# Performance work log

Hardware: AMD Instinct MI355X
Metric: run time of the kernel (lower is better)

## Reference

```python
import jax, jax.numpy as jnp
import numpy as np

ALPHA = 0.2  # LeakyReLU negative slope
NEG_BIG = -9e15

def setup_inputs() -> dict:
    key = jax.random.key(0)
    k1, k2, k3, k4 = jax.random.split(key, 4)
    N, F_IN, F_OUT = 8192, 128, 128
    h = jax.random.normal(k1, (N, F_IN), dtype=jnp.float32)
    adj = jax.random.randint(k2, (N, N), 0, 2, dtype=jnp.int32)
    # xavier-uniform-ish params
    W = jax.random.normal(k3, (F_IN, F_OUT), dtype=jnp.float32) * (1.0 / np.sqrt(F_IN))
    a = jax.random.normal(k4, (2 * F_OUT, 1), dtype=jnp.float32) * (1.0 / np.sqrt(2 * F_OUT))
    return {"h": h, "adj": adj, "W": W, "a": a}

def reference(h, adj, W, a):
    # Wh: [N, F_OUT]
    Wh = h @ W
    F_out = Wh.shape[1]
    # a_input @ a == (Wh @ a1)_i + (Wh @ a2)_j  (same math, no N^2*2F tensor)
    a1 = a[:F_out, 0]   # [F_OUT]
    a2 = a[F_out:, 0]   # [F_OUT]
    e = (Wh @ a1)[:, None] + (Wh @ a2)[None, :]        # [N, N]
    e = jnp.where(e >= 0, e, ALPHA * e)                # LeakyReLU(0.2)
    scores = jnp.where(adj > 0, e, NEG_BIG)
    attention = jax.nn.softmax(scores, axis=1)         # row-wise
    # dropout skipped (eval mode / training=False)
    return attention @ Wh                              # [N, F_OUT]
```

## Files before the change

kernel.cpp:

```cpp
#include <hip/hip_runtime.h>
#include <hip/hip_bf16.h>

#define N 8192
#define FD 128
#define LOG2E 1.4426950408889634f

typedef __attribute__((ext_vector_type(4))) float f4;
typedef __attribute__((ext_vector_type(4))) int i32x4;
typedef __attribute__((ext_vector_type(4))) unsigned int u32x4;
typedef __attribute__((ext_vector_type(8))) __bf16 bf16x8;

__device__ __forceinline__ unsigned short bfbits(float x){
  __bf16 b = (__bf16)x;
  return __builtin_bit_cast(unsigned short, b);
}

__global__ __launch_bounds__(256) void k12_wh(const float* __restrict__ h,
                                              const float* __restrict__ W,
                                              const float* __restrict__ a,
                                              unsigned short* __restrict__ Bsw,
                                              float* __restrict__ s1L,
                                              float* __restrict__ s2L){
  __shared__ float Wl[64*128];
  __shared__ float hT[128*33];
  int t = threadIdx.x;
  int i0 = blockIdx.x * 32;
  {
    int r  = t >> 3;
    int k0 = (t & 7) * 16;
    const f4* src = (const f4*)&h[(size_t)(i0 + r)*FD + k0];
    #pragma unroll
    for (int q = 0; q < 4; ++q){
      f4 v = src[q];
      #pragma unroll
      for (int e = 0; e < 4; ++e) hT[(k0 + q*4 + e)*33 + r] = v[e];
    }
  }
  int f0 = (t & 31) * 4;
  int r0 = (t >> 5) * 4;
  float acc[4][4] = {};
  for (int half = 0; half < 2; ++half){
    __syncthreads();
    #pragma unroll
    for (int v = 0; v < 8; ++v){
      int idx = (v*256 + t)*4;
      *(f4*)&Wl[idx] = *(const f4*)&W[half*8192 + idx];
    }
    __syncthreads();
    for (int k2 = 0; k2 < 64; ++k2){
      f4 wv = *(const f4*)&Wl[k2*FD + f0];
      f4 hv = *(const f4*)&hT[(half*64 + k2)*33 + r0];
      #pragma unroll
      for (int ri = 0; ri < 4; ++ri)
        #pragma unroll
        for (int fi = 0; fi < 4; ++fi)
          acc[ri][fi] = __builtin_fmaf(hv[ri], wv[fi], acc[ri][fi]);
    }
  }
  int jblk = blockIdx.x;
  int n  = f0 >> 4;
  int fl = f0 & 15;
  #pragma unroll
  for (int ri = 0; ri < 4; ++ri){
    int k = r0 + ri;
    size_t base = (((size_t)jblk*8 + n)*64 + ((k>>3)<<4))*8 + (k&7);
    #pragma unroll
    for (int fi = 0; fi < 4; ++fi)
      Bsw[base + (size_t)(fl + fi)*8] = bfbits(acc[ri][fi]);
  }
  f4 a1v = *(const f4*)&a[f0];
  f4 a2v = *(const f4*)&a[FD + f0];
  float p1[4], p2[4];
  #pragma unroll
  for (int ri = 0; ri < 4; ++ri){
    p1[ri] = 0.f; p2[ri] = 0.f;
    #pragma unroll
    for (int fi = 0; fi < 4; ++fi){
      p1[ri] = __builtin_fmaf(acc[ri][fi], a1v[fi], p1[ri]);
      p2[ri] = __builtin_fmaf(acc[ri][fi], a2v[fi], p2[ri]);
    }
  }
  #pragma unroll
  for (int d = 1; d < 32; d <<= 1){
    #pragma unroll
    for (int ri = 0; ri < 4; ++ri){
      p1[ri] += __shfl_xor(p1[ri], d, 32);
      p2[ri] += __shfl_xor(p2[ri], d, 32);
    }
  }
  if ((t & 31) == 0){
    #pragma unroll
    for (int ri = 0; ri < 4; ++ri){
      s1L[i0 + r0 + ri] = p1[ri] * LOG2E;
      s2L[i0 + r0 + ri] = p2[ri] * LOG2E;
    }
  }
}

__global__ __launch_bounds__(256) void k3_max(const float* __restrict__ s2L,
                                              float* __restrict__ M2L){
  __shared__ float red[4];
  int t = threadIdx.x;
  float m = -3.0e38f;
  for (int i = t; i < N; i += 256) m = fmaxf(m, s2L[i]);
  #pragma unroll
  for (int d = 1; d < 64; d <<= 1) m = fmaxf(m, __shfl_xor(m, d, 64));
  if ((t & 63) == 0) red[t >> 6] = m;
  __syncthreads();
  if (t == 0) *M2L = fmaxf(fmaxf(red[0], red[1]), fmaxf(red[2], red[3]));
}

__global__ __launch_bounds__(256,2) void k4_flash(const int* __restrict__ adj,
    const unsigned short* __restrict__ Bsw,
    const float* __restrict__ s1L, const float* __restrict__ s2L,
    const float* __restrict__ M2p,
    float* __restrict__ partial, float* __restrict__ denomp, int njc){
  __shared__ __align__(16) unsigned char bswl[2][32768];
  __shared__ __align__(16) unsigned char mknib[2][128*32];
  __shared__ __align__(16) float s2l[2][128];
  int t = threadIdx.x;
  int wv = t >> 6, lane = t & 63;
  int lrow = lane & 15, lgrp = lane >> 4;
  int bid = blockIdx.x;
  int y  = bid & (njc - 1);
  int bx = bid / njc;
  int jlen = N / njc;
  int jstart = y * jlen;
  int nmac = jlen >> 7;
  int rotm = nmac - 1;
  float M2 = *M2p;
  int i0w = bx*128 + wv*32;
  float s1a = s1L[i0w + lrow], s1b = s1L[i0w + 16 + lrow];
  float ea = s1a + M2, eb = s1b + M2;
  float maL = fmaxf(ea, 0.2f*ea);
  float mbL = fmaxf(eb, 0.2f*eb);

  f4 acc[2][8]; f4 accd[2];
  #pragma unroll
  for (int x = 0; x < 2; ++x){
    accd[x] = (f4){0.f,0.f,0.f,0.f};
    #pragma unroll
    for (int n = 0; n < 8; ++n) acc[x][n] = (f4){0.f,0.f,0.f,0.f};
  }
  u32x4 onesbits = (u32x4){0x3F803F80u,0x3F803F80u,0x3F803F80u,0x3F803F80u};
  bf16x8 ones = __builtin_bit_cast(bf16x8, onesbits);

  const i32x4* adj4 = (const i32x4*)adj;
  int sr2 = lane >> 5;
  int sj  = lane & 31;
  size_t abase = ((size_t)(bx*128 + wv*32 + sr2) * N) >> 2;

  i32x4 st[16];

  #define STAGE_BSW(jb0, b) do {                                               \
    const unsigned int* bg = (const unsigned int*)(Bsw + (size_t)((jb0) >> 5) * 4096); \
    _Pragma("unroll")                                                          \
    for (int q = 0; q < 8; ++q){                                               \
      int chunk = q*4 + wv;                                                    \
      __builtin_amdgcn_global_load_lds(                                        \
        (const __attribute__((address_space(1))) unsigned int*)(bg + (size_t)(chunk*64 + lane)*4), \
        (__attribute__((address_space(3))) unsigned int*)(&bswl[b][0] + chunk*1024), \
        16, 0, 0);                                                             \
    }                                                                          \
  } while(0)

  #define STAGE_ADJ(jb0) do {                                                  \
    size_t ab = abase + (size_t)((jb0) >> 2) + sj;                             \
    _Pragma("unroll")                                                          \
    for (int e = 0; e < 16; ++e) st[e] = adj4[ab + (size_t)e * 4096];          \
  } while(0)

  #define PACK_MASKS(b) do {                                                   \
    _Pragma("unroll")                                                          \
    for (int e = 0; e < 16; ++e){                                              \
      unsigned nib = (st[e][0] != 0 ? 1u : 0u) | (st[e][1] != 0 ? 2u : 0u)     \
                   | (st[e][2] != 0 ? 4u : 0u) | (st[e][3] != 0 ? 8u : 0u);    \
      int rloc = wv*32 + e*2 + sr2;                                            \
      mknib[b][rloc*32 + sj] = (unsigned char)nib;                             \
    }                                                                          \
  } while(0)

  int buf = 0;
  int jb_first = jstart + ((bx) & rotm) * 128;
  STAGE_BSW(jb_first, 0);
  STAGE_ADJ(jb_first);
  PACK_MASKS(0);
  if (t < 32) *(f4*)&s2l[0][t*4] = *(const f4*)&s2L[jb_first + t*4];
  __syncthreads();

  for (int m = 0; m < nmac; ++m){
    int jb0 = jstart + ((m + bx) & rotm) * 128;
    int jb1 = jstart + ((m + 1 + bx) & rotm) * 128;
    if (m + 1 < nmac){
      STAGE_BSW(jb1, buf ^ 1);
      STAGE_ADJ(jb1);
    }
    #pragma unroll
    for (int js = 0; js < 4; ++js){
      int jo = js*32 + lgrp*8;
      f4 ya = *(const f4*)&s2l[buf][jo];
      f4 yb = *(const f4*)&s2l[buf][jo+4];
      int gb = (js*4 + lgrp)*2;
      unsigned short ua = *(const unsigned short*)&mknib[buf][(wv*32 + lrow)*32 + gb];
      unsigned short ub = *(const unsigned short*)&mknib[buf][(wv*32 + 16 + lrow)*32 + gb];
      unsigned mba = (ua & 0xFu) | ((ua >> 4) & 0xF0u);
      unsigned mbb = (ub & 0xFu) | ((ub >> 4) & 0xF0u);
      bf16x8 fa, fb;
      #pragma unroll
      for (int e = 0; e < 8; ++e){
        float sjv = (e < 4) ? ya[e] : yb[e-4];
        float xa = s1a + sjv,            xb = s1b + sjv;
        float la = fmaxf(xa, 0.2f*xa),   lb = fmaxf(xb, 0.2f*xb);
        float pa = ((mba>>e)&1u) ? __builtin_amdgcn_exp2f(la - maL) : 0.f;
        float pb = ((mbb>>e)&1u) ? __builtin_amdgcn_exp2f(lb - mbL) : 0.f;
        fa[e] = (__bf16)pa; fb[e] = (__bf16)pb;
      }
      accd[0] = __builtin_amdgcn_mfma_f32_16x16x32_bf16(fa, ones, accd[0], 0, 0, 0);
      accd[1] = __builtin_amdgcn_mfma_f32_16x16x32_bf16(fb, ones, accd[1], 0, 0, 0);
      {
        u32x4 b0[4];
        #pragma unroll
        for (int n = 0; n < 4; ++n)
          b0[n] = *(const u32x4*)&bswl[buf][((js*8 + n)*64 + lane)*16];
        #pragma unroll
        for (int n = 0; n < 4; ++n){
          bf16x8 bb = __builtin_bit_cast(bf16x8, b0[n]);
          acc[0][n] = __builtin_amdgcn_mfma_f32_16x16x32_bf16(fa, bb, acc[0][n], 0, 0, 0);
          acc[1][n] = __builtin_amdgcn_mfma_f32_16x16x32_bf16(fb, bb, acc[1][n], 0, 0, 0);
        }
      }
      {
        u32x4 b1[4];
        #pragma unroll
        for (int n = 0; n < 4; ++n)
          b1[n] = *(const u32x4*)&bswl[buf][((js*8 + 4 + n)*64 + lane)*16];
        #pragma unroll
        for (int n = 0; n < 4; ++n){
          bf16x8 bb = __builtin_bit_cast(bf16x8, b1[n]);
          acc[0][4+n] = __builtin_amdgcn_mfma_f32_16x16x32_bf16(fa, bb, acc[0][4+n], 0, 0, 0);
          acc[1][4+n] = __builtin_amdgcn_mfma_f32_16x16x32_bf16(fb, bb, acc[1][4+n], 0, 0, 0);
        }
      }
    }
    if (m + 1 < nmac){
      PACK_MASKS(buf ^ 1);
      if (t < 32) *(f4*)&s2l[buf ^ 1][t*4] = *(const f4*)&s2L[jb1 + t*4];
    }
    __syncthreads();
    buf ^= 1;
  }

  if (lrow == 0){
    #pragma unroll
    for (int x = 0; x < 2; ++x)
      #pragma unroll
      for (int r = 0; r < 4; ++r)
        denomp[(size_t)y*N + i0w + x*16 + lgrp*4 + r] = accd[x][r];
  }
  float* pb = partial + (size_t)y * N * FD;
  #pragma unroll
  for (int x = 0; x < 2; ++x)
    #pragma unroll
    for (int n = 0; n < 8; ++n)
      #pragma unroll
      for (int r = 0; r < 4; ++r)
        pb[(size_t)(i0w + x*16 + lgrp*4 + r)*FD + n*16 + lrow] = acc[x][n][r];
}

__global__ __launch_bounds__(256) void k5_fin(const float* __restrict__ partial,
    const float* __restrict__ denomp, float* __restrict__ out, int njc){
  int g = blockIdx.x*256 + threadIdx.x;
  int i = g >> 7;
  float num = 0.f, den = 0.f;
  for (int c = 0; c < njc; ++c) num += partial[(size_t)c*N*FD + g];
  for (int c = 0; c < njc; ++c) den += denomp[(size_t)c*N + i];
  out[g] = num / den;
}

extern "C" void kernel_launch(void* const* d_in, const int* in_sizes, int n_in,
                              void* d_out, int out_size, void* d_ws, size_t ws_size,
                              hipStream_t stream){
  const float* h   = (const float*)d_in[0];
  const int*   adj = (const int*)d_in[1];
  const float* W   = (const float*)d_in[2];
  const float* a   = (const float*)d_in[3];
  float* out = (float*)d_out;
  char* ws = (char*)d_ws;

  unsigned short* Bsw = (unsigned short*)ws;
  float* s1L = (float*)(ws + (size_t)(6u<<20));
  float* s2L = (float*)(ws + (size_t)(6u<<20) + 32768);
  float* M2L = (float*)(ws + (size_t)(6u<<20) + 65536);
  float* denomp  = (float*)(ws + (size_t)(7u<<20));
  float* partial = (float*)(ws + (size_t)(8u<<20));

  size_t chunk = (size_t)N * FD * sizeof(float);
  int njc = 1;
  if (ws_size > ((size_t)(8u<<20))){
    size_t m = (ws_size - (size_t)(8u<<20)) / chunk;
    njc = (m >= 8) ? 8 : (m >= 4) ? 4 : (m >= 2) ? 2 : 1;
  }

  hipLaunchKernelGGL(k12_wh, dim3(256), dim3(256), 0, stream, h, W, a, Bsw, s1L, s2L);
  hipLaunchKernelGGL(k3_max, dim3(1),   dim3(256), 0, stream, s2L, M2L);
  hipLaunchKernelGGL(k4_flash, dim3(64*njc), dim3(256), 0, stream,
                     adj, Bsw, s1L, s2L, M2L, partial, denomp, njc);
  hipLaunchKernelGGL(k5_fin, dim3(N*FD/256), dim3(256), 0, stream, partial, denomp, out, njc);
}
```

Baseline: 392.3 us.

## Fuse max reduction and final normalization into neighbouring kernels via atomics

Drops the single-block max kernel. The projection kernel now folds each block's local max of s2 into a global atomicMax, using an order-preserving unsigned encoding of the float. Drops the separate finalize kernel too: in the flash kernel, the last of the 8 column-chunk blocks for a row tile (found with an atomic counter) sums the partials and denominators and writes the output. This removes two launches and the serial single-block reduction, but puts the reduction on only 64 blocks at the tail. It also hardcodes 8 column chunks and never resets the M2 atomic slot between calls.

```diff
diff --git a/kernel.cpp b/kernel.cpp
--- a/kernel.cpp
+++ b/kernel.cpp
@@ -20,11 +20,14 @@
                                               const float* __restrict__ a,
                                               unsigned short* __restrict__ Bsw,
                                               float* __restrict__ s1L,
-                                              float* __restrict__ s2L){
+                                              float* __restrict__ s2L,
+                                              unsigned* __restrict__ M2u,
+                                              int* __restrict__ ctr){
   __shared__ float Wl[64*128];
   __shared__ float hT[128*33];
   int t = threadIdx.x;
   int i0 = blockIdx.x * 32;
+  if (blockIdx.x == 0 && t < 64) ctr[t] = 0;
   {
     int r  = t >> 3;
     int k0 = (t & 7) * 16;
@@ -89,46 +92,43 @@
     }
   }
   if ((t & 31) == 0){
+    float lmax = -3.0e38f;
     #pragma unroll
     for (int ri = 0; ri < 4; ++ri){
-      s1L[i0 + r0 + ri] = p1[ri] * LOG2E;
-      s2L[i0 + r0 + ri] = p2[ri] * LOG2E;
-    }
-  }
-}
-
-__global__ __launch_bounds__(256) void k3_max(const float* __restrict__ s2L,
-                                              float* __restrict__ M2L){
-  __shared__ float red[4];
-  int t = threadIdx.x;
-  float m = -3.0e38f;
-  for (int i = t; i < N; i += 256) m = fmaxf(m, s2L[i]);
-  #pragma unroll
-  for (int d = 1; d < 64; d <<= 1) m = fmaxf(m, __shfl_xor(m, d, 64));
-  if ((t & 63) == 0) red[t >> 6] = m;
-  __syncthreads();
-  if (t == 0) *M2L = fmaxf(fmaxf(red[0], red[1]), fmaxf(red[2], red[3]));
+      float v1 = p1[ri] * LOG2E, v2 = p2[ri] * LOG2E;
+      s1L[i0 + r0 + ri] = v1;
+      s2L[i0 + r0 + ri] = v2;
+      lmax = fmaxf(lmax, v2);
+    }
+    unsigned b = __builtin_bit_cast(unsigned, lmax);
+    unsigned enc = (b >> 31) ? ~b : (b | 0x80000000u);
+    atomicMax(M2u, enc);
+  }
 }
 
 __global__ __launch_bounds__(256,2) void k4_flash(const int* __restrict__ adj,
     const unsigned short* __restrict__ Bsw,
     const float* __restrict__ s1L, const float* __restrict__ s2L,
-    const float* __restrict__ M2p,
-    float* __restrict__ partial, float* __restrict__ denomp, int njc){
+    const unsigned* __restrict__ M2u,
+    float* __restrict__ partial, float* __restrict__ denomp,
+    int* __restrict__ ctr, float* __restrict__ out){
   __shared__ __align__(16) unsigned char bswl[2][32768];
   __shared__ __align__(16) unsigned char mknib[2][128*32];
   __shared__ __align__(16) float s2l[2][128];
+  __shared__ float denl[128];
+  __shared__ int oldl;
   int t = threadIdx.x;
   int wv = t >> 6, lane = t & 63;
   int lrow = lane & 15, lgrp = lane >> 4;
   int bid = blockIdx.x;
-  int y  = bid & (njc - 1);
-  int bx = bid / njc;
-  int jlen = N / njc;
-  int jstart = y * jlen;
-  int nmac = jlen >> 7;
-  int rotm = nmac - 1;
-  float M2 = *M2p;
+  int y  = bid & 7;
+  int bx = bid >> 3;
+  int jstart = y * 1024;
+  const int nmac = 8;
+  const int rotm = nmac - 1;
+  unsigned mu = *M2u;
+  unsigned ub = (mu >> 31) ? (mu ^ 0x80000000u) : ~mu;
+  float M2 = __builtin_bit_cast(float, ub);
   int i0w = bx*128 + wv*32;
   float s1a = s1L[i0w + lrow], s1b = s1L[i0w + 16 + lrow];
   float ea = s1a + M2, eb = s1b + M2;
@@ -149,7 +149,6 @@
   int sr2 = lane >> 5;
   int sj  = lane & 31;
   size_t abase = ((size_t)(bx*128 + wv*32 + sr2) * N) >> 2;
-
   i32x4 st[16];
 
   #define STAGE_BSW(jb0, b) do {                                               \
@@ -181,7 +180,7 @@
   } while(0)
 
   int buf = 0;
-  int jb_first = jstart + ((bx) & rotm) * 128;
+  int jb_first = jstart + (bx & rotm) * 128;
   STAGE_BSW(jb_first, 0);
   STAGE_ADJ(jb_first);
   PACK_MASKS(0);
@@ -189,7 +188,6 @@
   __syncthreads();
 
   for (int m = 0; m < nmac; ++m){
-    int jb0 = jstart + ((m + bx) & rotm) * 128;
     int jb1 = jstart + ((m + 1 + bx) & rotm) * 128;
     if (m + 1 < nmac){
       STAGE_BSW(jb1, buf ^ 1);
@@ -202,9 +200,9 @@
       f4 yb = *(const f4*)&s2l[buf][jo+4];
       int gb = (js*4 + lgrp)*2;
       unsigned short ua = *(const unsigned short*)&mknib[buf][(wv*32 + lrow)*32 + gb];
-      unsigned short ub = *(const unsigned short*)&mknib[buf][(wv*32 + 16 + lrow)*32 + gb];
+      unsigned short ubm = *(const unsigned short*)&mknib[buf][(wv*32 + 16 + lrow)*32 + gb];
       unsigned mba = (ua & 0xFu) | ((ua >> 4) & 0xF0u);
-      unsigned mbb = (ub & 0xFu) | ((ub >> 4) & 0xF0u);
+      unsigned mbb = (ubm & 0xFu) | ((ubm >> 4) & 0xF0u);
       bf16x8 fa, fb;
       #pragma unroll
       for (int e = 0; e < 8; ++e){
@@ -265,16 +263,41 @@
       #pragma unroll
       for (int r = 0; r < 4; ++r)
         pb[(size_t)(i0w + x*16 + lgrp*4 + r)*FD + n*16 + lrow] = acc[x][n][r];
-}
-
-__global__ __launch_bounds__(256) void k5_fin(const float* __restrict__ partial,
-    const float* __restrict__ denomp, float* __restrict__ out, int njc){
-  int g = blockIdx.x*256 + threadIdx.x;
-  int i = g >> 7;
-  float num = 0.f, den = 0.f;
-  for (int c = 0; c < njc; ++c) num += partial[(size_t)c*N*FD + g];
-  for (int c = 0; c < njc; ++c) den += denomp[(size_t)c*N + i];
-  out[g] = num / den;
+
+  __threadfence();
+  __syncthreads();
+  if (t == 0)
+    oldl = __hip_atomic_fetch_add(&ctr[bx], 1, __ATOMIC_ACQ_REL, __HIP_MEMORY_SCOPE_AGENT);
+  __syncthreads();
+  if (oldl == 7){
+    __threadfence();
+    if (t < 128){
+      float s = 0.f;
+      #pragma unroll
+      for (int c = 0; c < 8; ++c) s += denomp[(size_t)c*N + bx*128 + t];
+      denl[t] = s;
+    }
+    __syncthreads();
+    const f4* p4 = (const f4*)partial;
+    f4* out4 = (f4*)out;
+    const size_t sl = (size_t)N*FD/4;
+    #pragma unroll
+    for (int q = 0; q < 16; ++q){
+      int idx = q*256 + t;
+      size_t g = (size_t)bx*4096 + idx;
+      f4 s = (f4){0.f,0.f,0.f,0.f};
+      #pragma unroll
+      for (int c = 0; c < 8; ++c){
+        f4 v = p4[(size_t)c*sl + g];
+        #pragma unroll
+        for (int e = 0; e < 4; ++e) s[e] += v[e];
+      }
+      float d = denl[idx >> 5];
+      #pragma unroll
+      for (int e = 0; e < 4; ++e) s[e] /= d;
+      out4[g] = s;
+    }
+  }
 }
 
 extern "C" void kernel_launch(void* const* d_in, const int* in_sizes, int n_in,
@@ -290,20 +313,13 @@
   unsigned short* Bsw = (unsigned short*)ws;
   float* s1L = (float*)(ws + (size_t)(6u<<20));
   float* s2L = (float*)(ws + (size_t)(6u<<20) + 32768);
-  float* M2L = (float*)(ws + (size_t)(6u<<20) + 65536);
+  unsigned* M2u = (unsigned*)(ws + (size_t)(6u<<20) + 65536);
+  int* ctr   = (int*)(ws + (size_t)(6u<<20) + 65600);
   float* denomp  = (float*)(ws + (size_t)(7u<<20));
   float* partial = (float*)(ws + (size_t)(8u<<20));
 
-  size_t chunk = (size_t)N * FD * sizeof(float);
-  int njc = 1;
-  if (ws_size > ((size_t)(8u<<20))){
-    size_t m = (ws_size - (size_t)(8u<<20)) / chunk;
-    njc = (m >= 8) ? 8 : (m >= 4) ? 4 : (m >= 2) ? 2 : 1;
-  }
-
-  hipLaunchKernelGGL(k12_wh, dim3(256), dim3(256), 0, stream, h, W, a, Bsw, s1L, s2L);
-  hipLaunchKernelGGL(k3_max, dim3(1),   dim3(256), 0, stream, s2L, M2L);
-  hipLaunchKernelGGL(k4_flash, dim3(64*njc), dim3(256), 0, stream,
-                     adj, Bsw, s1L, s2L, M2L, partial, denomp, njc);
-  hipLaunchKernelGGL(k5_fin, dim3(N*FD/256), dim3(256), 0, stream, partial, denomp, out, njc);
+  hipLaunchKernelGGL(k12_wh, dim3(256), dim3(256), 0, stream,
+                     h, W, a, Bsw, s1L, s2L, M2u, ctr);
+  hipLaunchKernelGGL(k4_flash, dim3(512), dim3(256), 0, stream,
+                     adj, Bsw, s1L, s2L, M2u, partial, denomp, ctr, out);
 }
```

Result: slower. 496.2 us (+26.5%).
